# Kernel tuning notes

Measured on AMD Instinct MI355X. Metric: run time of the kernel, lower is better.

Reference implementation:

```python
import jax, jax.numpy as jnp
import numpy as np

B, S, H = 1, 2048, 2048
NH, NKV, HD = 32, 8, 64
RBS, ICS, RBN = 64, 64, 16          # retrieval_block_size, input_chunk_size, retrieval_block_num
RLEN = RBS * RBN                     # 1024 retrieval tokens
KV = RLEN + S                        # 3072 total kv length
START = RLEN                         # INPUT_START_IDX
SCALE = HD ** -0.5
NEG = -1e9


def _document_ids():
    # mirrors get_document_ids
    ids = np.full(KV, -1, np.int32)
    ids[:START] = np.arange(START) // RBS + 1            # retrieval blocks -> 1..RBN
    chunk = np.arange(S) // ICS
    ids[START:] = np.where(chunk == 0, -1, np.minimum(chunk, RBN))
    return ids


def _block_mask():
    # mirrors causal_retrieval_mask_mod, precomputed dense [S, KV]
    ids = _document_ids()
    qpos = np.arange(S) + START
    kv = np.arange(KV)
    causal = (qpos[:, None] >= kv[None, :]) & (kv[None, :] > START)
    doc = (ids[qpos][:, None] == ids[None, :]) & (kv[None, :] < START)
    return jnp.asarray(causal | doc)


_MASK = _block_mask()


def _rotate_half(x):
    h = x.shape[-1] // 2
    return jnp.concatenate([-x[..., h:], x[..., :h]], axis=-1)


def setup_inputs() -> dict:
    key = jax.random.key(0)
    ks = jax.random.split(key, 6)
    inv_freq = 1.0 / (10000.0 ** (np.arange(0, HD, 2, dtype=np.float32) / HD))
    ang = np.arange(S, dtype=np.float32)[:, None] * inv_freq[None, :]   # [S, HD/2]
    emb = np.concatenate([ang, ang], axis=-1)                            # [S, HD]
    cos = jnp.asarray(np.cos(emb))[None].astype(jnp.float32)            # [1, S, HD]
    sin = jnp.asarray(np.sin(emb))[None].astype(jnp.float32)
    return {
        "hidden_states": jax.random.normal(ks[0], (B, S, H), jnp.float32),
        "cos": cos,
        "sin": sin,
        "retrieval_key": jax.random.normal(ks[1], (B, NKV, RLEN, HD), jnp.float32),
        "retrieval_value": jax.random.normal(ks[2], (B, NKV, RLEN, HD), jnp.float32),
        "Wq": jax.random.normal(ks[3], (H, NH * HD), jnp.float32) * 0.02,
        "Wk": jax.random.normal(ks[4], (H, NKV * HD), jnp.float32) * 0.02,
        "Wv": jax.random.normal(ks[5], (H, NKV * HD), jnp.float32) * 0.02,
        "Wo": jax.random.normal(jax.random.fold_in(key, 7), (NH * HD, H), jnp.float32) * 0.02,
    }


def reference(hidden_states, cos, sin, retrieval_key, retrieval_value, Wq, Wk, Wv, Wo):
    # QKV projections -> [B, nheads, S, HD]
    q = (hidden_states @ Wq).reshape(B, S, NH, HD).transpose(0, 2, 1, 3)
    k = (hidden_states @ Wk).reshape(B, S, NKV, HD).transpose(0, 2, 1, 3)
    v = (hidden_states @ Wv).reshape(B, S, NKV, HD).transpose(0, 2, 1, 3)
    # RoPE (retrieval kv is pre-encoded; rope only on current tokens)
    c, s = cos[:, None, :, :], sin[:, None, :, :]
    q = q * c + _rotate_half(q) * s
    k = k * c + _rotate_half(k) * s
    # prepend retrieval kv
    k = jnp.concatenate([retrieval_key, k], axis=2)    # [B, NKV, KV, HD]
    v = jnp.concatenate([retrieval_value, v], axis=2)
    # GQA: expand kv heads
    g = NH // NKV
    k = jnp.repeat(k, g, axis=1)                        # [B, NH, KV, HD]
    v = jnp.repeat(v, g, axis=1)
    scores = jnp.einsum("bhqd,bhkd->bhqk", q, k) * SCALE
    scores = jnp.where(_MASK[None, None], scores, NEG)
    probs = jax.nn.softmax(scores, axis=-1)
    # fully-masked rows (q_idx 0) -> zero output, matching flex_attention
    row_valid = _MASK.any(axis=-1)[None, None, :, None]
    probs = jnp.where(row_valid, probs, 0.0)
    out = jnp.einsum("bhqk,bhkd->bhqd", probs, v)
    out = out.transpose(0, 2, 1, 3).reshape(B, S, NH * HD)
    return out @ Wo
```

## Files before the change

### kernel.cpp

```cpp
#include <hip/hip_runtime.h>

#define S_LEN 2048
#define H_DIM 2048
#define NH 32
#define NKV 8
#define HD 64
#define RLEN 1024
#define KVTOT 3072
#define SCALE 0.125f
#define QS 0.18033688011112042f
#define FIX8 11.541560327111707f

typedef unsigned short ushort_t;
using short8 = __attribute__((ext_vector_type(8))) short;
using f32x4 = __attribute__((ext_vector_type(4))) float;

__device__ __forceinline__ float b2f(unsigned short u) {
    union { unsigned int i; float f; } v;
    v.i = ((unsigned int)u) << 16;
    return v.f;
}
__device__ __forceinline__ unsigned short f2b(float f) {
    union { float f; unsigned int i; } v;
    v.f = f;
    unsigned int x = v.i;
    return (unsigned short)((x + 0x7fffu + ((x >> 16) & 1u)) >> 16);
}

__global__ void detect9(const void* p0, const void* p1, const void* p2,
                        const void* p3, const void* p4, const void* p5,
                        const void* p6, const void* p7, const void* p8,
                        int* flags)
{
    __shared__ int bad;
    if (threadIdx.x == 0) bad = 0;
    __syncthreads();
    const void* ps[9] = {p0, p1, p2, p3, p4, p5, p6, p7, p8};
    const unsigned int* w = (const unsigned int*)ps[blockIdx.x];
    int cnt = 0;
    for (int i = threadIdx.x; i < 4096; i += blockDim.x) {
        unsigned int lo = w[i] & 0xFFFFu;
        unsigned int e = (lo >> 7) & 0xFFu;
        if (lo != 0u && (e < 90u || e > 140u)) ++cnt;
    }
    atomicAdd(&bad, cnt);
    __syncthreads();
    if (threadIdx.x == 0) flags[blockIdx.x] = (bad > 16) ? 1 : 0;
}

__global__ void cvt_b(const void* __restrict__ src, ushort_t* __restrict__ dst,
                      int n, const int* __restrict__ F_)
{
    const int F = *F_;
    int i = (blockIdx.x * 256 + threadIdx.x) * 8;
    if (i >= n) return;
    ushort_t o[8];
    if (F) {
        const float* p = (const float*)src + i;
        float4 f0 = ((const float4*)p)[0];
        float4 f1 = ((const float4*)p)[1];
        o[0] = f2b(f0.x); o[1] = f2b(f0.y); o[2] = f2b(f0.z); o[3] = f2b(f0.w);
        o[4] = f2b(f1.x); o[5] = f2b(f1.y); o[6] = f2b(f1.z); o[7] = f2b(f1.w);
        *(uint4*)(dst + i) = *(const uint4*)o;
    } else {
        *(uint4*)(dst + i) = *(const uint4*)((const ushort_t*)src + i);
    }
}

__global__ __launch_bounds__(256) void cvtW(
    const void* __restrict__ Wq, const void* __restrict__ Wk,
    const void* __restrict__ Wv, const void* __restrict__ Wo,
    ushort_t* __restrict__ WqkvT, ushort_t* __restrict__ WoT,
    const int* __restrict__ flags)
{
    const int z = blockIdx.z;
    if ((z == 1 || z == 2) && blockIdx.x >= 8) return;
    const void* src = (z == 0) ? Wq : (z == 1) ? Wk : (z == 2) ? Wv : Wo;
    const int F = flags[5 + z];
    const int C = (z == 1 || z == 2) ? 512 : 2048;
    ushort_t* dst = (z == 3) ? WoT : WqkvT;
    const int rofs = (z == 1) ? 2048 : (z == 2) ? 2560 : 0;

    __shared__ ushort_t S[64 * 72];
    const int r0 = blockIdx.y * 64, c0 = blockIdx.x * 64;
    const int lr = threadIdx.x >> 2, lc = (threadIdx.x & 3) * 16;
    ushort_t t[16];
    if (F) {
        const float* p = (const float*)src + (size_t)(r0 + lr) * C + c0 + lc;
#pragma unroll
        for (int j = 0; j < 16; j += 4) {
            float4 f = *(const float4*)(p + j);
            t[j] = f2b(f.x); t[j + 1] = f2b(f.y); t[j + 2] = f2b(f.z); t[j + 3] = f2b(f.w);
        }
    } else {
        const ushort_t* p = (const ushort_t*)src + (size_t)(r0 + lr) * C + c0 + lc;
        *(uint4*)t = ((const uint4*)p)[0];
        *(uint4*)(t + 8) = ((const uint4*)p)[1];
    }
    *(uint4*)&S[lr * 72 + lc] = *(const uint4*)t;
    *(uint4*)&S[lr * 72 + lc + 8] = *(const uint4*)(t + 8);
    __syncthreads();
    const int wc = threadIdx.x >> 2, wr = (threadIdx.x & 3) * 16;
    ushort_t o[16];
#pragma unroll
    for (int j = 0; j < 16; ++j) o[j] = S[(wr + j) * 72 + wc];
    ushort_t* q = dst + (size_t)(rofs + c0 + wc) * 2048 + r0 + wr;
    *(uint4*)q = *(const uint4*)o;
    *(uint4*)(q + 8) = *(const uint4*)(o + 8);
}

__global__ __launch_bounds__(256) void gemm_qkv(
    const ushort_t* __restrict__ A, const ushort_t* __restrict__ Bt,
    ushort_t* __restrict__ C, int N, int K)
{
    __shared__ __align__(16) ushort_t As[2][128 * 40];
    __shared__ __align__(16) ushort_t Bs[2][128 * 40];
    const int tid = threadIdx.x;
    const int wave = tid >> 6, lane = tid & 63;
    const int lq = lane & 15, quad = lane >> 4;
    const int m0 = blockIdx.y * 128, n0 = blockIdx.x * 128;
    const int wm = (wave & 1) * 64, wn = (wave >> 1) * 64;
    const int sr = tid >> 1, sk = (tid & 1) * 16;
    const int nk = K >> 5;

    f32x4 acc[4][4];
#pragma unroll
    for (int i = 0; i < 4; ++i)
#pragma unroll
        for (int j = 0; j < 4; ++j) acc[i][j] = (f32x4){0.f, 0.f, 0.f, 0.f};

    const ushort_t* ap = A + (size_t)(m0 + sr) * K + sk;
    const ushort_t* bp = Bt + (size_t)(n0 + sr) * K + sk;
    {
        uint4 a0 = ((const uint4*)ap)[0], a1 = ((const uint4*)ap)[1];
        uint4 b0 = ((const uint4*)bp)[0], b1 = ((const uint4*)bp)[1];
        *(uint4*)&As[0][sr * 40 + sk] = a0; *(uint4*)&As[0][sr * 40 + sk + 8] = a1;
        *(uint4*)&Bs[0][sr * 40 + sk] = b0; *(uint4*)&Bs[0][sr * 40 + sk + 8] = b1;
    }

    for (int kt = 0; kt < nk; ++kt) {
        const int cur = kt & 1;
        uint4 na0, na1, nb0, nb1;
        const bool more = (kt + 1 < nk);
        if (more) {
            const ushort_t* ap2 = ap + (kt + 1) * 32;
            const ushort_t* bp2 = bp + (kt + 1) * 32;
            na0 = ((const uint4*)ap2)[0]; na1 = ((const uint4*)ap2)[1];
            nb0 = ((const uint4*)bp2)[0]; nb1 = ((const uint4*)bp2)[1];
        }
        __syncthreads();
        short8 afr[4], bfr[4];
#pragma unroll
        for (int i = 0; i < 4; ++i)
            afr[i] = *(const short8*)&As[cur][(wm + i * 16 + lq) * 40 + quad * 8];
#pragma unroll
        for (int j = 0; j < 4; ++j)
            bfr[j] = *(const short8*)&Bs[cur][(wn + j * 16 + lq) * 40 + quad * 8];
#pragma unroll
        for (int i = 0; i < 4; ++i)
#pragma unroll
            for (int j = 0; j < 4; ++j)
                acc[i][j] = __builtin_amdgcn_mfma_f32_16x16x32_bf16(afr[i], bfr[j], acc[i][j], 0, 0, 0);
        __syncthreads();
        if (more) {
            const int nxt = cur ^ 1;
            *(uint4*)&As[nxt][sr * 40 + sk] = na0; *(uint4*)&As[nxt][sr * 40 + sk + 8] = na1;
            *(uint4*)&Bs[nxt][sr * 40 + sk] = nb0; *(uint4*)&Bs[nxt][sr * 40 + sk + 8] = nb1;
        }
    }

#pragma unroll
    for (int i = 0; i < 4; ++i)
#pragma unroll
        for (int r = 0; r < 4; ++r) {
            ushort_t* cp = C + (size_t)(m0 + wm + i * 16 + quad * 4 + r) * N + n0 + wn + lq;
#pragma unroll
            for (int j = 0; j < 4; ++j) cp[j * 16] = f2b(acc[i][j][r]);
        }
}

__global__ __launch_bounds__(256) void gemm_fin(
    const ushort_t* __restrict__ A, const ushort_t* __restrict__ Bt,
    void* __restrict__ Cv, int N, int K, const int* __restrict__ oF_)
{
    const int oF = *oF_;
    __shared__ __align__(16) ushort_t As[2][128 * 40];
    __shared__ __align__(16) ushort_t Bs[2][128 * 40];
    const int tid = threadIdx.x;
    const int wave = tid >> 6, lane = tid & 63;
    const int lq = lane & 15, quad = lane >> 4;
    const int m0 = blockIdx.y * 128, n0 = blockIdx.x * 128;
    const int wm = (wave & 1) * 64, wn = (wave >> 1) * 64;
    const int sr = tid >> 1, sk = (tid & 1) * 16;
    const int nk = K >> 5;

    f32x4 acc[4][4];
#pragma unroll
    for (int i = 0; i < 4; ++i)
#pragma unroll
        for (int j = 0; j < 4; ++j) acc[i][j] = (f32x4){0.f, 0.f, 0.f, 0.f};

    const ushort_t* ap = A + (size_t)(m0 + sr) * K + sk;
    const ushort_t* bp = Bt + (size_t)(n0 + sr) * K + sk;
    {
        uint4 a0 = ((const uint4*)ap)[0], a1 = ((const uint4*)ap)[1];
        uint4 b0 = ((const uint4*)bp)[0], b1 = ((const uint4*)bp)[1];
        *(uint4*)&As[0][sr * 40 + sk] = a0; *(uint4*)&As[0][sr * 40 + sk + 8] = a1;
        *(uint4*)&Bs[0][sr * 40 + sk] = b0; *(uint4*)&Bs[0][sr * 40 + sk + 8] = b1;
    }

    for (int kt = 0; kt < nk; ++kt) {
        const int cur = kt & 1;
        uint4 na0, na1, nb0, nb1;
        const bool more = (kt + 1 < nk);
        if (more) {
            const ushort_t* ap2 = ap + (kt + 1) * 32;
            const ushort_t* bp2 = bp + (kt + 1) * 32;
            na0 = ((const uint4*)ap2)[0]; na1 = ((const uint4*)ap2)[1];
            nb0 = ((const uint4*)bp2)[0]; nb1 = ((const uint4*)bp2)[1];
        }
        __syncthreads();
        short8 afr[4], bfr[4];
#pragma unroll
        for (int i = 0; i < 4; ++i)
            afr[i] = *(const short8*)&As[cur][(wm + i * 16 + lq) * 40 + quad * 8];
#pragma unroll
        for (int j = 0; j < 4; ++j)
            bfr[j] = *(const short8*)&Bs[cur][(wn + j * 16 + lq) * 40 + quad * 8];
#pragma unroll
        for (int i = 0; i < 4; ++i)
#pragma unroll
            for (int j = 0; j < 4; ++j)
                acc[i][j] = __builtin_amdgcn_mfma_f32_16x16x32_bf16(afr[i], bfr[j], acc[i][j], 0, 0, 0);
        __syncthreads();
        if (more) {
            const int nxt = cur ^ 1;
            *(uint4*)&As[nxt][sr * 40 + sk] = na0; *(uint4*)&As[nxt][sr * 40 + sk + 8] = na1;
            *(uint4*)&Bs[nxt][sr * 40 + sk] = nb0; *(uint4*)&Bs[nxt][sr * 40 + sk + 8] = nb1;
        }
    }

#pragma unroll
    for (int i = 0; i < 4; ++i)
#pragma unroll
        for (int r = 0; r < 4; ++r) {
            size_t off = (size_t)(m0 + wm + i * 16 + quad * 4 + r) * N + n0 + wn + lq;
            if (oF) {
                float* cp = (float*)Cv + off;
#pragma unroll
                for (int j = 0; j < 4; ++j) cp[j * 16] = acc[i][j][r];
            } else {
                ushort_t* cp = (ushort_t*)Cv + off;
#pragma unroll
                for (int j = 0; j < 4; ++j) cp[j * 16] = f2b(acc[i][j][r]);
            }
        }
}

__global__ __launch_bounds__(256) void prepKV(
    const void* __restrict__ rk, const void* __restrict__ rv,
    const ushort_t* __restrict__ qkvp,
    const void* __restrict__ cosv, const void* __restrict__ sinv,
    ushort_t* __restrict__ ktall, ushort_t* __restrict__ vtall,
    const int* __restrict__ flags)
{
    if (blockIdx.z == 0) {
        const int vF = flags[4];
        const int t = blockIdx.x;
        const int kvh = blockIdx.y;
        __shared__ ushort_t S[64 * 72];
        const int lr = threadIdx.x >> 2, lc = (threadIdx.x & 3) * 16;
        ushort_t tt[16];
        if (t < 16) {
            size_t base = ((size_t)kvh * RLEN + t * 64 + lr) * HD + lc;
            if (vF) {
                const float* p = (const float*)rv + base;
#pragma unroll
                for (int j = 0; j < 16; j += 4) {
                    float4 f = *(const float4*)(p + j);
                    tt[j] = f2b(f.x); tt[j + 1] = f2b(f.y); tt[j + 2] = f2b(f.z); tt[j + 3] = f2b(f.w);
                }
            } else {
                const ushort_t* p = (const ushort_t*)rv + base;
                *(uint4*)tt = ((const uint4*)p)[0];
                *(uint4*)(tt + 8) = ((const uint4*)p)[1];
            }
        } else {
            const ushort_t* p = qkvp + (size_t)((t - 16) * 64 + lr) * 3072 + 2560 + kvh * HD + lc;
            *(uint4*)tt = ((const uint4*)p)[0];
            *(uint4*)(tt + 8) = ((const uint4*)p)[1];
        }
        *(uint4*)&S[lr * 72 + lc] = *(const uint4*)tt;
        *(uint4*)&S[lr * 72 + lc + 8] = *(const uint4*)(tt + 8);
        __syncthreads();
        const int wc = threadIdx.x >> 2, wr = (threadIdx.x & 3) * 16;
        ushort_t o[16];
#pragma unroll
        for (int j = 0; j < 16; ++j) o[j] = S[(wr + j) * 72 + wc];
        const int blk = t * 2 + (wr >> 5);
        ushort_t* q = vtall + (((size_t)(kvh * 96 + blk) * 64 + wc) * 32) + (wr & 31);
        *(uint4*)q = *(const uint4*)o;
        *(uint4*)(q + 8) = *(const uint4*)(o + 8);
    } else {
        const int kF = flags[3], cF = flags[1], sF = flags[2];
        int flat = (blockIdx.y * 48 + blockIdx.x) * 256 + threadIdx.x;
        const int d0 = (flat & 3) * 8;
        const int p = (flat >> 2) % KVTOT;
        const int kvh = (flat >> 2) / KVTOT;
        ushort_t o0[8], o1[8];
        if (p < RLEN) {
            size_t base = ((size_t)kvh * RLEN + p) * HD;
            if (kF) {
                const float* s = (const float*)rk + base;
#pragma unroll
                for (int j = 0; j < 8; j += 4) {
                    float4 f = *(const float4*)(s + d0 + j);
                    o0[j] = f2b(f.x); o0[j + 1] = f2b(f.y); o0[j + 2] = f2b(f.z); o0[j + 3] = f2b(f.w);
                    float4 g = *(const float4*)(s + d0 + 32 + j);
                    o1[j] = f2b(g.x); o1[j + 1] = f2b(g.y); o1[j + 2] = f2b(g.z); o1[j + 3] = f2b(g.w);
                }
            } else {
                const ushort_t* s = (const ushort_t*)rk + base;
                *(uint4*)o0 = *(const uint4*)(s + d0);
                *(uint4*)o1 = *(const uint4*)(s + d0 + 32);
            }
        } else {
            const int si = p - RLEN;
            const ushort_t* s = qkvp + (size_t)si * 3072 + 2048 + kvh * HD;
            uint4 u0 = *(const uint4*)(s + d0);
            uint4 u1 = *(const uint4*)(s + d0 + 32);
            const ushort_t* a16 = (const ushort_t*)&u0;
            const ushort_t* b16 = (const ushort_t*)&u1;
            int ci = si * HD + d0;
            float c0[8], c1[8], s0[8], s1[8];
            if (cF) {
                const float* cp = (const float*)cosv + ci;
#pragma unroll
                for (int j = 0; j < 8; ++j) { c0[j] = cp[j]; c1[j] = cp[j + 32]; }
            } else {
                const ushort_t* cp = (const ushort_t*)cosv + ci;
#pragma unroll
                for (int j = 0; j < 8; ++j) { c0[j] = b2f(cp[j]); c1[j] = b2f(cp[j + 32]); }
            }
            if (sF) {
                const float* sp = (const float*)sinv + ci;
#pragma unroll
                for (int j = 0; j < 8; ++j) { s0[j] = sp[j]; s1[j] = sp[j + 32]; }
            } else {
                const ushort_t* sp = (const ushort_t*)sinv + ci;
#pragma unroll
                for (int j = 0; j < 8; ++j) { s0[j] = b2f(sp[j]); s1[j] = b2f(sp[j + 32]); }
            }
#pragma unroll
            for (int j = 0; j < 8; ++j) {
                float a = b2f(a16[j]), b = b2f(b16[j]);
                o0[j] = f2b(a * c0[j] - b * s0[j]);
                o1[j] = f2b(b * c1[j] + a * s1[j]);
            }
        }
        ushort_t* q = ktall + ((size_t)kvh * KVTOT + p) * HD;
        *(uint4*)(q + d0) = *(const uint4*)o0;
        *(uint4*)(q + d0 + 32) = *(const uint4*)o1;
    }
}

__global__ __launch_bounds__(256) void fattn(
    const ushort_t* __restrict__ qkvp, const ushort_t* __restrict__ ktall,
    const ushort_t* __restrict__ vtall, ushort_t* __restrict__ attno,
    const void* __restrict__ cosv, const void* __restrict__ sinv,
    const int* __restrict__ flags)
{
    const int cF = flags[1], sF = flags[2];
    const int h = blockIdx.x;
    const int qb = 31 - blockIdx.y;
    const int kvh = h >> 2;
    const int tid = threadIdx.x;
    const int wave = tid >> 6;
    const int lane = tid & 63;
    const int lq = lane & 15;
    const int quad = lane >> 4;
    const int rb64 = ((qb < 17 ? qb : 16) - 1) * 64;

    __shared__ __align__(16) ushort_t Ks[128 * 72];
    __shared__ __align__(16) ushort_t Vt[64 * 136];
    __shared__ __align__(16) ushort_t Ps[4 * 16 * 136];
    ushort_t* pw = &Ps[wave * 16 * 136];

    short8 qfrag[2];
    {
        const int row_g = qb * 64 + wave * 16 + lq;
        const ushort_t* qrow = qkvp + (size_t)row_g * 3072 + h * HD;
        short8 t0 = *(const short8*)(qrow + quad * 8);
        short8 t1 = *(const short8*)(qrow + 32 + quad * 8);
        const int ci = row_g * HD + quad * 8;
        float c0[8], c1[8], s0[8], s1[8];
        if (cF) {
            const float* cp = (const float*)cosv + ci;
#pragma unroll
            for (int j = 0; j < 8; ++j) { c0[j] = cp[j]; c1[j] = cp[j + 32]; }
        } else {
            const ushort_t* cp = (const ushort_t*)cosv + ci;
#pragma unroll
            for (int j = 0; j < 8; ++j) { c0[j] = b2f(cp[j]); c1[j] = b2f(cp[j + 32]); }
        }
        if (sF) {
            const float* sp = (const float*)sinv + ci;
#pragma unroll
            for (int j = 0; j < 8; ++j) { s0[j] = sp[j]; s1[j] = sp[j + 32]; }
        } else {
            const ushort_t* sp = (const ushort_t*)sinv + ci;
#pragma unroll
            for (int j = 0; j < 8; ++j) { s0[j] = b2f(sp[j]); s1[j] = b2f(sp[j + 32]); }
        }
#pragma unroll
        for (int j = 0; j < 8; ++j) {
            float a = b2f((unsigned short)t0[j]), b = b2f((unsigned short)t1[j]);
            qfrag[0][j] = (short)f2b((a * c0[j] - b * s0[j]) * QS);
            qfrag[1][j] = (short)f2b((b * c1[j] + a * s1[j]) * QS);
        }
    }

    f32x4 oacc[4];
#pragma unroll
    for (int nt = 0; nt < 4; ++nt) oacc[nt] = (f32x4){0.f, 0.f, 0.f, 0.f};
    float lsum[4] = {0.f, 0.f, 0.f, 0.f};

    const int Lq = (qb > 0) ? qb * 64 + 128 : 64;
    const int nch = (Lq + 127) >> 7;
    const ushort_t* kbase = ktall + (size_t)kvh * KVTOT * HD;
    const ushort_t* vbase = vtall + (size_t)kvh * 96 * 2048;

    for (int c = 0; c < nch; ++c) {
        {
            const int row = tid >> 1;
            const int d0 = (tid & 1) * 32;
            int p = c * 128 + row;
            uint4 z = {0, 0, 0, 0};
            uint4 k0 = z, k1 = z, k2 = z, k3 = z;
            if (p < Lq) {
                int pk = (qb > 0) ? ((p < 64) ? rb64 + p : 960 + p) : RLEN + p;
                const uint4* s = (const uint4*)(kbase + (size_t)pk * HD + d0);
                k0 = s[0]; k1 = s[1]; k2 = s[2]; k3 = s[3];
            }
            uint4* dk = (uint4*)&Ks[row * 72 + d0];
            dk[0] = k0; dk[1] = k1; dk[2] = k2; dk[3] = k3;
        }
        {
            const int dd = tid >> 2;
            const int vb = tid & 3;
            int p = c * 128 + vb * 32;
            uint4 z = {0, 0, 0, 0};
            uint4 v0 = z, v1 = z, v2 = z, v3 = z;
            if (p < Lq) {
                int pk = (qb > 0) ? ((p < 64) ? rb64 + p : 960 + p) : RLEN + p;
                const uint4* s = (const uint4*)(vbase + ((size_t)(pk >> 5) * 64 + dd) * 32);
                v0 = s[0]; v1 = s[1]; v2 = s[2]; v3 = s[3];
            }
            uint4* dv = (uint4*)&Vt[dd * 136 + vb * 32];
            dv[0] = v0; dv[1] = v1; dv[2] = v2; dv[3] = v3;
        }
        __syncthreads();

        const bool lastc = (c == nch - 1) || (qb == 0);
#pragma unroll
        for (int nt = 0; nt < 8; ++nt) {
            f32x4 a = (f32x4){0.f, 0.f, 0.f, 0.f};
            a = __builtin_amdgcn_mfma_f32_16x16x32_bf16(qfrag[0],
                *(const short8*)&Ks[(nt * 16 + lq) * 72 + quad * 8], a, 0, 0, 0);
            a = __builtin_amdgcn_mfma_f32_16x16x32_bf16(qfrag[1],
                *(const short8*)&Ks[(nt * 16 + lq) * 72 + 32 + quad * 8], a, 0, 0, 0);
            const int p = c * 128 + nt * 16 + lq;
#pragma unroll
            for (int r = 0; r < 4; ++r) {
                float pexp = exp2f(a[r] - FIX8);
                if (lastc) {
                    const int qg = qb * 64 + wave * 16 + quad * 4 + r;
                    bool valid;
                    if (qb > 0) valid = (p < 64) || ((p - 64) >= 1 && (p - 64) <= qg);
                    else        valid = (p >= 1 && p <= qg);
                    if (!valid) pexp = 0.f;
                } else if (c == 0) {
                    if (p == 64) pexp = 0.f;
                }
                lsum[r] += pexp;
                pw[(quad * 4 + r) * 136 + nt * 16 + lq] = f2b(pexp);
            }
        }

#pragma unroll
        for (int kc = 0; kc < 4; ++kc) {
            short8 pa = *(const short8*)&pw[lq * 136 + kc * 32 + quad * 8];
#pragma unroll
            for (int ntd = 0; ntd < 4; ++ntd)
                oacc[ntd] = __builtin_amdgcn_mfma_f32_16x16x32_bf16(pa,
                    *(const short8*)&Vt[(ntd * 16 + lq) * 136 + kc * 32 + quad * 8],
                    oacc[ntd], 0, 0, 0);
        }
        __syncthreads();
    }

#pragma unroll
    for (int r = 0; r < 4; ++r) {
        float v = lsum[r];
        v += __shfl_xor(v, 1, 64); v += __shfl_xor(v, 2, 64);
        v += __shfl_xor(v, 4, 64); v += __shfl_xor(v, 8, 64);
        lsum[r] = v;
    }
#pragma unroll
    for (int r = 0; r < 4; ++r) {
        const int qg = qb * 64 + wave * 16 + quad * 4 + r;
        const float inv = (qg == 0) ? 0.f : 1.f / lsum[r];
        ushort_t* orow = attno + (size_t)qg * 2048 + h * HD;
#pragma unroll
        for (int nt = 0; nt < 4; ++nt)
            orow[nt * 16 + lq] = f2b(oacc[nt][r] * inv);
    }
}

extern "C" void kernel_launch(void* const* d_in, const int* in_sizes, int n_in,
                              void* d_out, int out_size, void* d_ws, size_t ws_size,
                              hipStream_t stream) {
    const void* hs   = d_in[0];
    const void* cosv = d_in[1];
    const void* sinv = d_in[2];
    const void* rk   = d_in[3];
    const void* rv   = d_in[4];
    const void* Wq   = d_in[5];
    const void* Wk   = d_in[6];
    const void* Wv   = d_in[7];
    const void* Wo   = d_in[8];

    char* ws = (char*)d_ws;
    int*      flags  = (int*)ws;
    ushort_t* hsb    = (ushort_t*)(ws + (1u  << 20));
    ushort_t* ktall  = hsb;
    ushort_t* vtall  = (ushort_t*)(ws + (1u << 20) + (13u << 18));
    ushort_t* WqkvT  = (ushort_t*)(ws + (9u  << 20));
    ushort_t* attno  = WqkvT;
    ushort_t* WoT    = (ushort_t*)(ws + (21u << 20));
    ushort_t* qkvp   = (ushort_t*)(ws + (29u << 20));

    detect9<<<9, 256, 0, stream>>>(hs, cosv, sinv, rk, rv, Wq, Wk, Wv, Wo, flags);

    cvt_b<<<(H_DIM * S_LEN / 8 + 255) / 256, 256, 0, stream>>>(hs, hsb, H_DIM * S_LEN, flags + 0);
    cvtW<<<dim3(32, 32, 4), 256, 0, stream>>>(Wq, Wk, Wv, Wo, WqkvT, WoT, flags);

    gemm_qkv<<<dim3(3072 / 128, 2048 / 128), 256, 0, stream>>>(hsb, WqkvT, qkvp, 3072, 2048);

    prepKV<<<dim3(48, 8, 2), 256, 0, stream>>>(rk, rv, qkvp, cosv, sinv, ktall, vtall, flags);

    fattn<<<dim3(NH, 32), 256, 0, stream>>>(qkvp, ktall, vtall, attno, cosv, sinv, flags);

    gemm_fin<<<dim3(2048 / 128, 2048 / 128), 256, 0, stream>>>(attno, WoT, d_out, 2048, 2048, flags + 0);
}
```

Baseline: 274.2 us.

## Shrink GEMM M-tile to 64 and load V fragments directly from global in attention

New measurement: 270.9 us. Within noise of the previous version (-1.2%).

```diff
diff --git a/kernel.cpp b/kernel.cpp
--- a/kernel.cpp
+++ b/kernel.cpp
@@ -113,64 +113,64 @@
     const ushort_t* __restrict__ A, const ushort_t* __restrict__ Bt,
     ushort_t* __restrict__ C, int N, int K)
 {
-    __shared__ __align__(16) ushort_t As[2][128 * 40];
+    __shared__ __align__(16) ushort_t As[2][64 * 40];
     __shared__ __align__(16) ushort_t Bs[2][128 * 40];
     const int tid = threadIdx.x;
     const int wave = tid >> 6, lane = tid & 63;
     const int lq = lane & 15, quad = lane >> 4;
-    const int m0 = blockIdx.y * 128, n0 = blockIdx.x * 128;
-    const int wm = (wave & 1) * 64, wn = (wave >> 1) * 64;
-    const int sr = tid >> 1, sk = (tid & 1) * 16;
+    const int m0 = blockIdx.y * 64, n0 = blockIdx.x * 128;
+    const int wm = (wave & 1) * 32, wn = (wave >> 1) * 64;
+    const int ar = tid >> 2, ak = (tid & 3) * 8;
+    const int br = tid >> 1, bk = (tid & 1) * 16;
     const int nk = K >> 5;
 
-    f32x4 acc[4][4];
-#pragma unroll
-    for (int i = 0; i < 4; ++i)
+    f32x4 acc[2][4];
+#pragma unroll
+    for (int i = 0; i < 2; ++i)
 #pragma unroll
         for (int j = 0; j < 4; ++j) acc[i][j] = (f32x4){0.f, 0.f, 0.f, 0.f};
 
-    const ushort_t* ap = A + (size_t)(m0 + sr) * K + sk;
-    const ushort_t* bp = Bt + (size_t)(n0 + sr) * K + sk;
+    const ushort_t* ap = A + (size_t)(m0 + ar) * K + ak;
+    const ushort_t* bp = Bt + (size_t)(n0 + br) * K + bk;
     {
-        uint4 a0 = ((const uint4*)ap)[0], a1 = ((const uint4*)ap)[1];
+        uint4 a0 = ((const uint4*)ap)[0];
         uint4 b0 = ((const uint4*)bp)[0], b1 = ((const uint4*)bp)[1];
-        *(uint4*)&As[0][sr * 40 + sk] = a0; *(uint4*)&As[0][sr * 40 + sk + 8] = a1;
-        *(uint4*)&Bs[0][sr * 40 + sk] = b0; *(uint4*)&Bs[0][sr * 40 + sk + 8] = b1;
+        *(uint4*)&As[0][ar * 40 + ak] = a0;
+        *(uint4*)&Bs[0][br * 40 + bk] = b0; *(uint4*)&Bs[0][br * 40 + bk + 8] = b1;
     }
 
     for (int kt = 0; kt < nk; ++kt) {
         const int cur = kt & 1;
-        uint4 na0, na1, nb0, nb1;
+        uint4 na0, nb0, nb1;
         const bool more = (kt + 1 < nk);
         if (more) {
-            const ushort_t* ap2 = ap + (kt + 1) * 32;
+            na0 = *(const uint4*)(ap + (kt + 1) * 32);
             const ushort_t* bp2 = bp + (kt + 1) * 32;
-            na0 = ((const uint4*)ap2)[0]; na1 = ((const uint4*)ap2)[1];
             nb0 = ((const uint4*)bp2)[0]; nb1 = ((const uint4*)bp2)[1];
         }
         __syncthreads();
-        short8 afr[4], bfr[4];
-#pragma unroll
-        for (int i = 0; i < 4; ++i)
+        short8 afr[2], bfr[4];
+#pragma unroll
+        for (int i = 0; i < 2; ++i)
             afr[i] = *(const short8*)&As[cur][(wm + i * 16 + lq) * 40 + quad * 8];
 #pragma unroll
         for (int j = 0; j < 4; ++j)
             bfr[j] = *(const short8*)&Bs[cur][(wn + j * 16 + lq) * 40 + quad * 8];
 #pragma unroll
-        for (int i = 0; i < 4; ++i)
+        for (int i = 0; i < 2; ++i)
 #pragma unroll
             for (int j = 0; j < 4; ++j)
                 acc[i][j] = __builtin_amdgcn_mfma_f32_16x16x32_bf16(afr[i], bfr[j], acc[i][j], 0, 0, 0);
         __syncthreads();
         if (more) {
             const int nxt = cur ^ 1;
-            *(uint4*)&As[nxt][sr * 40 + sk] = na0; *(uint4*)&As[nxt][sr * 40 + sk + 8] = na1;
-            *(uint4*)&Bs[nxt][sr * 40 + sk] = nb0; *(uint4*)&Bs[nxt][sr * 40 + sk + 8] = nb1;
-        }
-    }
-
-#pragma unroll
-    for (int i = 0; i < 4; ++i)
+            *(uint4*)&As[nxt][ar * 40 + ak] = na0;
+            *(uint4*)&Bs[nxt][br * 40 + bk] = nb0; *(uint4*)&Bs[nxt][br * 40 + bk + 8] = nb1;
+        }
+    }
+
+#pragma unroll
+    for (int i = 0; i < 2; ++i)
 #pragma unroll
         for (int r = 0; r < 4; ++r) {
             ushort_t* cp = C + (size_t)(m0 + wm + i * 16 + quad * 4 + r) * N + n0 + wn + lq;
@@ -184,64 +184,64 @@
     void* __restrict__ Cv, int N, int K, const int* __restrict__ oF_)
 {
     const int oF = *oF_;
-    __shared__ __align__(16) ushort_t As[2][128 * 40];
+    __shared__ __align__(16) ushort_t As[2][64 * 40];
     __shared__ __align__(16) ushort_t Bs[2][128 * 40];
     const int tid = threadIdx.x;
     const int wave = tid >> 6, lane = tid & 63;
     const int lq = lane & 15, quad = lane >> 4;
-    const int m0 = blockIdx.y * 128, n0 = blockIdx.x * 128;
-    const int wm = (wave & 1) * 64, wn = (wave >> 1) * 64;
-    const int sr = tid >> 1, sk = (tid & 1) * 16;
+    const int m0 = blockIdx.y * 64, n0 = blockIdx.x * 128;
+    const int wm = (wave & 1) * 32, wn = (wave >> 1) * 64;
+    const int ar = tid >> 2, ak = (tid & 3) * 8;
+    const int br = tid >> 1, bk = (tid & 1) * 16;
     const int nk = K >> 5;
 
-    f32x4 acc[4][4];
-#pragma unroll
-    for (int i = 0; i < 4; ++i)
+    f32x4 acc[2][4];
+#pragma unroll
+    for (int i = 0; i < 2; ++i)
 #pragma unroll
         for (int j = 0; j < 4; ++j) acc[i][j] = (f32x4){0.f, 0.f, 0.f, 0.f};
 
-    const ushort_t* ap = A + (size_t)(m0 + sr) * K + sk;
-    const ushort_t* bp = Bt + (size_t)(n0 + sr) * K + sk;
+    const ushort_t* ap = A + (size_t)(m0 + ar) * K + ak;
+    const ushort_t* bp = Bt + (size_t)(n0 + br) * K + bk;
     {
-        uint4 a0 = ((const uint4*)ap)[0], a1 = ((const uint4*)ap)[1];
+        uint4 a0 = ((const uint4*)ap)[0];
         uint4 b0 = ((const uint4*)bp)[0], b1 = ((const uint4*)bp)[1];
-        *(uint4*)&As[0][sr * 40 + sk] = a0; *(uint4*)&As[0][sr * 40 + sk + 8] = a1;
-        *(uint4*)&Bs[0][sr * 40 + sk] = b0; *(uint4*)&Bs[0][sr * 40 + sk + 8] = b1;
+        *(uint4*)&As[0][ar * 40 + ak] = a0;
+        *(uint4*)&Bs[0][br * 40 + bk] = b0; *(uint4*)&Bs[0][br * 40 + bk + 8] = b1;
     }
 
     for (int kt = 0; kt < nk; ++kt) {
         const int cur = kt & 1;
-        uint4 na0, na1, nb0, nb1;
+        uint4 na0, nb0, nb1;
         const bool more = (kt + 1 < nk);
         if (more) {
-            const ushort_t* ap2 = ap + (kt + 1) * 32;
+            na0 = *(const uint4*)(ap + (kt + 1) * 32);
             const ushort_t* bp2 = bp + (kt + 1) * 32;
-            na0 = ((const uint4*)ap2)[0]; na1 = ((const uint4*)ap2)[1];
             nb0 = ((const uint4*)bp2)[0]; nb1 = ((const uint4*)bp2)[1];
         }
         __syncthreads();
-        short8 afr[4], bfr[4];
-#pragma unroll
-        for (int i = 0; i < 4; ++i)
+        short8 afr[2], bfr[4];
+#pragma unroll
+        for (int i = 0; i < 2; ++i)
             afr[i] = *(const short8*)&As[cur][(wm + i * 16 + lq) * 40 + quad * 8];
 #pragma unroll
         for (int j = 0; j < 4; ++j)
             bfr[j] = *(const short8*)&Bs[cur][(wn + j * 16 + lq) * 40 + quad * 8];
 #pragma unroll
-        for (int i = 0; i < 4; ++i)
+        for (int i = 0; i < 2; ++i)
 #pragma unroll
             for (int j = 0; j < 4; ++j)
                 acc[i][j] = __builtin_amdgcn_mfma_f32_16x16x32_bf16(afr[i], bfr[j], acc[i][j], 0, 0, 0);
         __syncthreads();
         if (more) {
             const int nxt = cur ^ 1;
-            *(uint4*)&As[nxt][sr * 40 + sk] = na0; *(uint4*)&As[nxt][sr * 40 + sk + 8] = na1;
-            *(uint4*)&Bs[nxt][sr * 40 + sk] = nb0; *(uint4*)&Bs[nxt][sr * 40 + sk + 8] = nb1;
-        }
-    }
-
-#pragma unroll
-    for (int i = 0; i < 4; ++i)
+            *(uint4*)&As[nxt][ar * 40 + ak] = na0;
+            *(uint4*)&Bs[nxt][br * 40 + bk] = nb0; *(uint4*)&Bs[nxt][br * 40 + bk + 8] = nb1;
+        }
+    }
+
+#pragma unroll
+    for (int i = 0; i < 2; ++i)
 #pragma unroll
         for (int r = 0; r < 4; ++r) {
             size_t off = (size_t)(m0 + wm + i * 16 + quad * 4 + r) * N + n0 + wn + lq;
@@ -382,7 +382,6 @@
     const int rb64 = ((qb < 17 ? qb : 16) - 1) * 64;
 
     __shared__ __align__(16) ushort_t Ks[128 * 72];
-    __shared__ __align__(16) ushort_t Vt[64 * 136];
     __shared__ __align__(16) ushort_t Ps[4 * 16 * 136];
     ushort_t* pw = &Ps[wave * 16 * 136];
 
@@ -431,33 +430,38 @@
     const ushort_t* vbase = vtall + (size_t)kvh * 96 * 2048;
 
     for (int c = 0; c < nch; ++c) {
+        uint4 kreg0, kreg1, kreg2, kreg3;
+        const int krow = tid >> 1;
+        const int kd0 = (tid & 1) * 32;
         {
-            const int row = tid >> 1;
-            const int d0 = (tid & 1) * 32;
-            int p = c * 128 + row;
+            int p = c * 128 + krow;
             uint4 z = {0, 0, 0, 0};
-            uint4 k0 = z, k1 = z, k2 = z, k3 = z;
+            kreg0 = z; kreg1 = z; kreg2 = z; kreg3 = z;
             if (p < Lq) {
                 int pk = (qb > 0) ? ((p < 64) ? rb64 + p : 960 + p) : RLEN + p;
-                const uint4* s = (const uint4*)(kbase + (size_t)pk * HD + d0);
-                k0 = s[0]; k1 = s[1]; k2 = s[2]; k3 = s[3];
-            }
-            uint4* dk = (uint4*)&Ks[row * 72 + d0];
-            dk[0] = k0; dk[1] = k1; dk[2] = k2; dk[3] = k3;
-        }
+                const uint4* s = (const uint4*)(kbase + (size_t)pk * HD + kd0);
+                kreg0 = s[0]; kreg1 = s[1]; kreg2 = s[2]; kreg3 = s[3];
+            }
+        }
+        int vblk[4];
+#pragma unroll
+        for (int kc = 0; kc < 4; ++kc) {
+            int p = c * 128 + kc * 32;
+            int pk = (qb > 0) ? ((p < 64) ? rb64 + p : 960 + p) : RLEN + p;
+            if (pk > KVTOT - 1) pk = KVTOT - 1;
+            vblk[kc] = pk >> 5;
+        }
+        short8 vfA[4], vfB[4];
+#pragma unroll
+        for (int ntd = 0; ntd < 4; ++ntd)
+            vfA[ntd] = *(const short8*)(vbase + ((size_t)vblk[0] * 64 + ntd * 16 + lq) * 32 + quad * 8);
+#pragma unroll
+        for (int ntd = 0; ntd < 4; ++ntd)
+            vfB[ntd] = *(const short8*)(vbase + ((size_t)vblk[1] * 64 + ntd * 16 + lq) * 32 + quad * 8);
+
         {
-            const int dd = tid >> 2;
-            const int vb = tid & 3;
-            int p = c * 128 + vb * 32;
-            uint4 z = {0, 0, 0, 0};
-            uint4 v0 = z, v1 = z, v2 = z, v3 = z;
-            if (p < Lq) {
-                int pk = (qb > 0) ? ((p < 64) ? rb64 + p : 960 + p) : RLEN + p;
-                const uint4* s = (const uint4*)(vbase + ((size_t)(pk >> 5) * 64 + dd) * 32);
-                v0 = s[0]; v1 = s[1]; v2 = s[2]; v3 = s[3];
-            }
-            uint4* dv = (uint4*)&Vt[dd * 136 + vb * 32];
-            dv[0] = v0; dv[1] = v1; dv[2] = v2; dv[3] = v3;
+            uint4* dk = (uint4*)&Ks[krow * 72 + kd0];
+            dk[0] = kreg0; dk[1] = kreg1; dk[2] = kreg2; dk[3] = kreg3;
         }
         __syncthreads();
 
@@ -490,11 +494,20 @@
 #pragma unroll
         for (int kc = 0; kc < 4; ++kc) {
             short8 pa = *(const short8*)&pw[lq * 136 + kc * 32 + quad * 8];
-#pragma unroll
-            for (int ntd = 0; ntd < 4; ++ntd)
-                oacc[ntd] = __builtin_amdgcn_mfma_f32_16x16x32_bf16(pa,
-                    *(const short8*)&Vt[(ntd * 16 + lq) * 136 + kc * 32 + quad * 8],
-                    oacc[ntd], 0, 0, 0);
+            short8 vf0, vf1, vf2, vf3;
+            if (kc == 0)      { vf0 = vfA[0]; vf1 = vfA[1]; vf2 = vfA[2]; vf3 = vfA[3]; }
+            else if (kc == 1) { vf0 = vfB[0]; vf1 = vfB[1]; vf2 = vfB[2]; vf3 = vfB[3]; }
+            else {
+                const int b = vblk[kc];
+                vf0 = *(const short8*)(vbase + ((size_t)b * 64 + 0 * 16 + lq) * 32 + quad * 8);
+                vf1 = *(const short8*)(vbase + ((size_t)b * 64 + 1 * 16 + lq) * 32 + quad * 8);
+                vf2 = *(const short8*)(vbase + ((size_t)b * 64 + 2 * 16 + lq) * 32 + quad * 8);
+                vf3 = *(const short8*)(vbase + ((size_t)b * 64 + 3 * 16 + lq) * 32 + quad * 8);
+            }
+            oacc[0] = __builtin_amdgcn_mfma_f32_16x16x32_bf16(pa, vf0, oacc[0], 0, 0, 0);
+            oacc[1] = __builtin_amdgcn_mfma_f32_16x16x32_bf16(pa, vf1, oacc[1], 0, 0, 0);
+            oacc[2] = __builtin_amdgcn_mfma_f32_16x16x32_bf16(pa, vf2, oacc[2], 0, 0, 0);
+            oacc[3] = __builtin_amdgcn_mfma_f32_16x16x32_bf16(pa, vf3, oacc[3], 0, 0, 0);
         }
         __syncthreads();
     }
@@ -545,11 +558,11 @@
     cvt_b<<<(H_DIM * S_LEN / 8 + 255) / 256, 256, 0, stream>>>(hs, hsb, H_DIM * S_LEN, flags + 0);
     cvtW<<<dim3(32, 32, 4), 256, 0, stream>>>(Wq, Wk, Wv, Wo, WqkvT, WoT, flags);
 
-    gemm_qkv<<<dim3(3072 / 128, 2048 / 128), 256, 0, stream>>>(hsb, WqkvT, qkvp, 3072, 2048);
+    gemm_qkv<<<dim3(3072 / 128, 2048 / 64), 256, 0, stream>>>(hsb, WqkvT, qkvp, 3072, 2048);
 
     prepKV<<<dim3(48, 8, 2), 256, 0, stream>>>(rk, rv, qkvp, cosv, sinv, ktall, vtall, flags);
 
     fattn<<<dim3(NH, 32), 256, 0, stream>>>(qkvp, ktall, vtall, attno, cosv, sinv, flags);
 
-    gemm_fin<<<dim3(2048 / 128, 2048 / 128), 256, 0, stream>>>(attno, WoT, d_out, 2048, 2048, flags + 0);
-}
+    gemm_fin<<<dim3(2048 / 128, 2048 / 64), 256, 0, stream>>>(attno, WoT, d_out, 2048, 2048, flags + 0);
+}
```
